# Performance work log

Hardware: AMD Instinct MI355X
Metric: run time of the kernel (lower is better)

Reference implementation:

```python
import jax, jax.numpy as jnp
import numpy as np

BATCH_SIZE = 1024  # init kwarg: Pair(batch_size)
D = 260            # per-item feature dim; last 4 entries are (x1, y1, x2, y2)


def setup_inputs() -> dict:
    key = jax.random.key(0)
    k_feat, k_xy, k_wh = jax.random.split(key, 3)
    feats = jax.random.normal(k_feat, (1, BATCH_SIZE, D - 4), dtype=jnp.float32)
    # Valid boxes: x2 > x1, y2 > y1 so areas are strictly positive (avoids div-by-zero,
    # matching the intended use on real detector boxes).
    xy1 = jax.random.uniform(k_xy, (1, BATCH_SIZE, 2), minval=0.0, maxval=0.5)
    wh = jax.random.uniform(k_wh, (1, BATCH_SIZE, 2), minval=0.05, maxval=0.5)
    bbox = jnp.concatenate([xy1, xy1 + wh], axis=-1)  # (x1, y1, x2, y2)
    inputs = jnp.concatenate([feats, bbox], axis=-1).astype(jnp.float32)
    return {"inputs": inputs}


def reference(inputs) -> jnp.ndarray:
    n = inputs.shape[1] // 2          # loops run over range(batch_size // 2)
    d = inputs.shape[2]
    x = inputs[0, :n]                 # [n, D] — only first half of rows is used
    x1, y1, x2, y2 = x[:, -4], x[:, -3], x[:, -2], x[:, -1]
    area = (x2 - x1) * (y2 - y1)      # [n]
    # Pairwise intersection, all (i, j) at once.
    w = jnp.maximum(0.0, jnp.minimum(x2[:, None], x2[None, :]) - jnp.maximum(x1[:, None], x1[None, :]))
    h = jnp.maximum(0.0, jnp.minimum(y2[:, None], y2[None, :]) - jnp.maximum(y1[:, None], y1[None, :]))
    inter = w * h                     # [n, n]
    r1 = inter / area[:, None]        # intersection / area_i
    r2 = inter / area[None, :]        # intersection / area_j
    xi = jnp.broadcast_to(x[:, None, :], (n, n, d))  # features of i
    xj = jnp.broadcast_to(x[None, :, :], (n, n, d))  # features of j
    out = jnp.concatenate([xi, xj, r1[..., None], r2[..., None]], axis=-1)  # [n, n, 2D+2]
    # Original appends in i-outer, j-inner order then concats on axis 1.
    return out.reshape(1, n * n, 2 * d + 2)
```

## Files before the change

### kernel.cpp

```cpp
#include <hip/hip_runtime.h>


#define N 512
#define D 260
#define JT 32

__global__ __launch_bounds__(256) void pair_kernel(const float* __restrict__ in,
                                                   float* __restrict__ out) {
    const int b    = blockIdx.x;
    const int i    = b >> 4;
    const int j0   = (b & 15) * JT;
    const int tid  = threadIdx.x;
    const int lane = tid & 63;
    const int w    = tid >> 6;

    __shared__ float2 s_xj[JT * 130];
    __shared__ float  s_r1[JT], s_r2[JT];

    const float* rowi = in + i * D;
    const float2 xi_a = *(const float2*)(rowi + 2 * lane);
    const float2 xi_b = *(const float2*)(rowi + 128 + 2 * lane);
    const float4 bb   = *(const float4*)(rowi + 256);

    const float2* gj2 = (const float2*)(in + (size_t)j0 * D);
    for (int t = tid; t < JT * 130; t += 256) s_xj[t] = gj2[t];

    if (tid < JT) {
        const float* bj = in + (size_t)(j0 + tid) * D + 256;
        const float x1j = bj[0], y1j = bj[1], x2j = bj[2], y2j = bj[3];
        const float x1i = bb.x, y1i = bb.y, x2i = bb.z, y2i = bb.w;
        float ww = fmaxf(0.0f, fminf(x2i, x2j) - fmaxf(x1i, x1j));
        float hh = fmaxf(0.0f, fminf(y2i, y2j) - fmaxf(y1i, y1j));
        const float inter = ww * hh;
        s_r1[tid] = inter / ((x2i - x1i) * (y2i - y1i));
        s_r2[tid] = inter / ((x2j - x1j) * (y2j - y1j));
    }
    __syncthreads();

    for (int lj = w; lj < JT; lj += 4) {
        float2* ob = (float2*)(out + (size_t)(i * N + j0 + lj) * 522);
        const float2* xr = &s_xj[lj * 130];

        const int idx2 = (lane < 2) ? 0 : (lane - 2);
        float2 v2 = xr[idx2];
        if (lane == 0) v2 = make_float2(bb.x, bb.y);
        if (lane == 1) v2 = make_float2(bb.z, bb.w);
        const float2 v3 = xr[62 + lane];

        ob[lane]       = xi_a;
        ob[64 + lane]  = xi_b;
        ob[128 + lane] = v2;
        ob[192 + lane] = v3;
        if (lane < 5) {
            const float2 v4 = (lane < 4) ? xr[126 + ((lane < 4) ? lane : 3)]
                                         : make_float2(s_r1[lj], s_r2[lj]);
            ob[256 + lane] = v4;
        }
    }
}

extern "C" void kernel_launch(void* const* d_in, const int* in_sizes, int n_in,
                              void* d_out, int out_size, void* d_ws, size_t ws_size,
                              hipStream_t stream) {
    const float* in = (const float*)d_in[0];
    float* out = (float*)d_out;
    pair_kernel<<<N * (N / JT), 256, 0, stream>>>(in, out);
}
```

Baseline: 537.9 us.

## Stage full output rows in shared memory and write them with float4 stores

Each block now builds its entire contiguous output region (16 pair rows of 522 floats) in shared memory, including the box-overlap ratios, then copies it to global memory with fully coalesced 16-byte stores. Before, the kernel issued scattered float2 stores per row with partial-wave tails. The j-tile shrinks from 32 to 16 so the image fits in shared memory, which doubles the block count and adds an extra shared-memory round trip.

Result: no change. 530.0 us (-1.5%).

```diff
diff --git a/kernel.cpp b/kernel.cpp
--- a/kernel.cpp
+++ b/kernel.cpp
@@ -3,60 +3,61 @@
 
 #define N 512
 #define D 260
-#define JT 32
+#define JT 16
+#define ROW 522
+#define REG_F4 (JT * ROW / 4)
 
 __global__ __launch_bounds__(256) void pair_kernel(const float* __restrict__ in,
                                                    float* __restrict__ out) {
     const int b    = blockIdx.x;
-    const int i    = b >> 4;
-    const int j0   = (b & 15) * JT;
+    const int i    = b >> 5;
+    const int j0   = (b & 31) * JT;
     const int tid  = threadIdx.x;
     const int lane = tid & 63;
     const int w    = tid >> 6;
 
-    __shared__ float2 s_xj[JT * 130];
-    __shared__ float  s_r1[JT], s_r2[JT];
+    __shared__ __align__(16) float s_img[JT * ROW];
 
     const float* rowi = in + i * D;
-    const float2 xi_a = *(const float2*)(rowi + 2 * lane);
-    const float2 xi_b = *(const float2*)(rowi + 128 + 2 * lane);
+    const float2 xi_a = ((const float2*)rowi)[lane];
+    const float2 xi_b = ((const float2*)rowi)[64 + lane];
     const float4 bb   = *(const float4*)(rowi + 256);
 
-    const float2* gj2 = (const float2*)(in + (size_t)j0 * D);
-    for (int t = tid; t < JT * 130; t += 256) s_xj[t] = gj2[t];
+    for (int lj = w; lj < JT; lj += 4) {
+        const float* xjrow = in + (size_t)(j0 + lj) * D;
+        const float2 ga = ((const float2*)xjrow)[lane];
+        const float2 gb = ((const float2*)xjrow)[64 + lane];
+        float2* row2 = (float2*)(s_img + lj * ROW);
 
-    if (tid < JT) {
-        const float* bj = in + (size_t)(j0 + tid) * D + 256;
-        const float x1j = bj[0], y1j = bj[1], x2j = bj[2], y2j = bj[3];
-        const float x1i = bb.x, y1i = bb.y, x2i = bb.z, y2i = bb.w;
-        float ww = fmaxf(0.0f, fminf(x2i, x2j) - fmaxf(x1i, x1j));
-        float hh = fmaxf(0.0f, fminf(y2i, y2j) - fmaxf(y1i, y1j));
-        const float inter = ww * hh;
-        s_r1[tid] = inter / ((x2i - x1i) * (y2i - y1i));
-        s_r2[tid] = inter / ((x2j - x1j) * (y2j - y1j));
+        row2[lane]       = xi_a;
+        row2[64 + lane]  = xi_b;
+        row2[130 + lane] = ga;
+        row2[194 + lane] = gb;
+        if (lane < 2) {
+            row2[128 + lane] = lane ? make_float2(bb.z, bb.w)
+                                    : make_float2(bb.x, bb.y);
+            row2[258 + lane] = ((const float2*)xjrow)[128 + lane];
+        }
+        if (lane == 2) {
+            const float4 bj = *(const float4*)(xjrow + 256);
+            const float ww = fmaxf(0.0f, fminf(bb.z, bj.z) - fmaxf(bb.x, bj.x));
+            const float hh = fmaxf(0.0f, fminf(bb.w, bj.w) - fmaxf(bb.y, bj.y));
+            const float inter = ww * hh;
+            row2[260] = make_float2(inter / ((bb.z - bb.x) * (bb.w - bb.y)),
+                                    inter / ((bj.z - bj.x) * (bj.w - bj.y)));
+        }
     }
     __syncthreads();
 
-    for (int lj = w; lj < JT; lj += 4) {
-        float2* ob = (float2*)(out + (size_t)(i * N + j0 + lj) * 522);
-        const float2* xr = &s_xj[lj * 130];
+    const float4* s4 = (const float4*)s_img;
+    float4* o4 = (float4*)(out + (size_t)(i * N + j0) * ROW);
 
-        const int idx2 = (lane < 2) ? 0 : (lane - 2);
-        float2 v2 = xr[idx2];
-        if (lane == 0) v2 = make_float2(bb.x, bb.y);
-        if (lane == 1) v2 = make_float2(bb.z, bb.w);
-        const float2 v3 = xr[62 + lane];
-
-        ob[lane]       = xi_a;
-        ob[64 + lane]  = xi_b;
-        ob[128 + lane] = v2;
-        ob[192 + lane] = v3;
-        if (lane < 5) {
-            const float2 v4 = (lane < 4) ? xr[126 + ((lane < 4) ? lane : 3)]
-                                         : make_float2(s_r1[lj], s_r2[lj]);
-            ob[256 + lane] = v4;
-        }
+    int t = tid;
+    #pragma unroll
+    for (int k = 0; k < 8; ++k, t += 256) {
+        o4[t] = s4[t];
     }
+    if (t < REG_F4) o4[t] = s4[t];
 }
 
 extern "C" void kernel_launch(void* const* d_in, const int* in_sizes, int n_in,
```
